# Kernel optimization log

Hardware: AMD Instinct MI355X
Metric: run time of the kernel (lower is better)

Reference implementation:

```python
import jax, jax.numpy as jnp
import numpy as np

EPS = 1e-8  # matches torch F.cosine_similarity eps


def setup_inputs() -> dict:
    key = jax.random.key(0)
    k1, k2, k3 = jax.random.split(key, 3)
    S, B, H = 16, 512, 2048
    OGLogits = jax.random.normal(k1, (B, H), dtype=jnp.float32)
    enhancedSamplesLogits = jax.random.normal(k2, (S, B, H), dtype=jnp.float32)
    W = jax.random.normal(k3, (H, H), dtype=jnp.float32) * (1.0 / np.sqrt(H))
    b = jnp.zeros((H,), dtype=jnp.float32)
    return {"OGLogits": OGLogits, "enhancedSamplesLogits": enhancedSamplesLogits, "W": W, "b": b}


def reference(OGLogits, enhancedSamplesLogits, W, b):
    # Original torch code builds the full (S*B, B) cosine-similarity matrix and
    # keeps only the diagonal via an eye mask; mathematically that equals the
    # per-pair cosine similarity cos(enhanced[s,b], OG[b]), computed directly here.
    e_norm = jnp.linalg.norm(enhancedSamplesLogits, axis=-1)          # (S, B)
    o_norm = jnp.linalg.norm(OGLogits, axis=-1)                       # (B,)
    dots = jnp.einsum('sbh,bh->sb', enhancedSamplesLogits, OGLogits)  # (S, B)
    sims = dots / jnp.maximum(e_norm * o_norm[None, :], EPS)          # (S, B)
    weighted = enhancedSamplesLogits * sims[..., None]                # (S, B, H)
    weightedRep = weighted.mean(axis=0)                               # (B, H)
    return weightedRep @ W.T + b                                      # (B, H)
```

## Files before the change

kernel.cpp:

```cpp
#include <hip/hip_runtime.h>

#define S_DIM 16
#define B_DIM 512
#define H_DIM 2048
#define EPS 1e-8f

typedef short bf16x8 __attribute__((ext_vector_type(8)));
typedef float f32x16 __attribute__((ext_vector_type(16)));

__device__ __forceinline__ unsigned short f2bf(float f) {
    union { float f; unsigned int u; } v; v.f = f;
    unsigned int u = v.u;
    unsigned int r = (u + 0x7fffu + ((u >> 16) & 1u)) >> 16;
    return (unsigned short)r;
}

__device__ __forceinline__ float dot4(const float4& a, const float4& b) {
    return a.x*b.x + a.y*b.y + a.z*b.z + a.w*b.w;
}

__global__ __launch_bounds__(512, 4) void fused_kernel(
    const float* __restrict__ OG, const float* __restrict__ E,
    const float* __restrict__ W, unsigned short* __restrict__ wrep,
    unsigned short* __restrict__ Wb) {
    const int b = blockIdx.x;
    const int t = threadIdx.x;
    const int lane = t & 63;
    const int wave = t >> 6;

    __shared__ float4 buf[8][512];
    __shared__ float4 ogs[512];
    __shared__ float red[8];

    const float4* w4 = (const float4*)W;
    ushort4* wb4 = (ushort4*)Wb;
    const size_t wbase = (size_t)b * 2048 + t;

    float4 wv0 = w4[wbase];
    float4 wv1 = w4[wbase + 512];
    const float4* og4 = (const float4*)(OG + (size_t)b * H_DIM);
    float4 o = og4[t];

    const float4* e4a = (const float4*)(E + ((size_t)wave * B_DIM + b) * H_DIM);
    const float4* e4b = (const float4*)(E + ((size_t)(wave + 8) * B_DIM + b) * H_DIM);
    float4 ea[8], eb[8];
    #pragma unroll
    for (int i = 0; i < 8; ++i) {
        ea[i] = e4a[i * 64 + lane];
        eb[i] = e4b[i * 64 + lane];
    }
    float4 wv2 = w4[wbase + 1024];
    float4 wv3 = w4[wbase + 1536];

    ogs[t] = o;
    float p = dot4(o, o);
    #pragma unroll
    for (int m = 32; m >= 1; m >>= 1) p += __shfl_xor(p, m, 64);
    if (lane == 0) red[wave] = p;

    {
        ushort4 c0, c1;
        c0.x = f2bf(wv0.x); c0.y = f2bf(wv0.y); c0.z = f2bf(wv0.z); c0.w = f2bf(wv0.w);
        c1.x = f2bf(wv1.x); c1.y = f2bf(wv1.y); c1.z = f2bf(wv1.z); c1.w = f2bf(wv1.w);
        wb4[wbase] = c0;
        wb4[wbase + 512] = c1;
    }
    __syncthreads();

    float og2 = 0.f;
    #pragma unroll
    for (int w = 0; w < 8; ++w) og2 += red[w];
    const float onorm = sqrtf(og2);

    float da = 0.f, na = 0.f, db = 0.f, nb = 0.f;
    #pragma unroll
    for (int i = 0; i < 8; ++i) {
        float4 g = ogs[i * 64 + lane];
        da += dot4(ea[i], g); na += dot4(ea[i], ea[i]);
        db += dot4(eb[i], g); nb += dot4(eb[i], eb[i]);
    }
    #pragma unroll
    for (int m = 32; m >= 1; m >>= 1) {
        da += __shfl_xor(da, m, 64);
        na += __shfl_xor(na, m, 64);
        db += __shfl_xor(db, m, 64);
        nb += __shfl_xor(nb, m, 64);
    }
    const float sima = da / fmaxf(sqrtf(na) * onorm, EPS);
    const float simb = db / fmaxf(sqrtf(nb) * onorm, EPS);

    #pragma unroll
    for (int i = 0; i < 8; ++i) {
        float4 v;
        v.x = ea[i].x * sima + eb[i].x * simb;
        v.y = ea[i].y * sima + eb[i].y * simb;
        v.z = ea[i].z * sima + eb[i].z * simb;
        v.w = ea[i].w * sima + eb[i].w * simb;
        buf[wave][i * 64 + lane] = v;
    }
    {
        ushort4 c2, c3;
        c2.x = f2bf(wv2.x); c2.y = f2bf(wv2.y); c2.z = f2bf(wv2.z); c2.w = f2bf(wv2.w);
        c3.x = f2bf(wv3.x); c3.y = f2bf(wv3.y); c3.z = f2bf(wv3.z); c3.w = f2bf(wv3.w);
        wb4[wbase + 1024] = c2;
        wb4[wbase + 1536] = c3;
    }
    __syncthreads();

    float4 s = buf[0][t];
    #pragma unroll
    for (int w = 1; w < 8; ++w) {
        float4 v = buf[w][t];
        s.x += v.x; s.y += v.y; s.z += v.z; s.w += v.w;
    }
    const float sc = 1.f / (float)S_DIM;
    ushort4 ob;
    ob.x = f2bf(s.x * sc); ob.y = f2bf(s.y * sc);
    ob.z = f2bf(s.z * sc); ob.w = f2bf(s.w * sc);
    ((ushort4*)wrep)[(size_t)b * (H_DIM / 4) + t] = ob;
}

__global__ __launch_bounds__(256) void gemm_kernel(
    const unsigned short* __restrict__ A, const unsigned short* __restrict__ Wb,
    const float* __restrict__ bias, float* __restrict__ out) {
    const int bid = blockIdx.x;
    const int m0 = (bid & 7) * 64;
    const int n0 = (bid >> 3) * 64;

    __shared__ unsigned short As[2][64 * 72];
    __shared__ unsigned short Bs[2][64 * 72];

    const int t = threadIdx.x;
    const int lane = t & 63;
    const int wave = t >> 6;
    const int wm = (wave & 1) * 32;
    const int wn = (wave >> 1) * 32;

    const int lr = t >> 2, lq = t & 3;
    const unsigned short* ap = A  + (size_t)(m0 + lr) * H_DIM + lq * 16;
    const unsigned short* bp = Wb + (size_t)(n0 + lr) * H_DIM + lq * 16;

    const int sw = (lr & 7) << 4;
    const int w0 = lr * 72 + (((lq * 32) ^ sw) >> 1);
    const int w1 = lr * 72 + (((lq * 32 + 16) ^ sw) >> 1);

    f32x16 acc0 = {0.f,0.f,0.f,0.f,0.f,0.f,0.f,0.f,
                   0.f,0.f,0.f,0.f,0.f,0.f,0.f,0.f};
    f32x16 acc1 = {0.f,0.f,0.f,0.f,0.f,0.f,0.f,0.f,
                   0.f,0.f,0.f,0.f,0.f,0.f,0.f,0.f};

    const int row = lane & 31;
    const int hi = lane >> 5;
    const int rbase = (wm + row) * 72;
    const int rsw = ((row & 7) << 4);
    int roffA[4], roffB[4];
    #pragma unroll
    for (int ks = 0; ks < 4; ++ks) {
        const int x = (ks * 32 + hi * 16) ^ rsw;
        roffA[ks] = rbase + (x >> 1);
        roffB[ks] = (wn + row) * 72 + (x >> 1);
    }

    uint4 ra0 = *(const uint4*)(ap);
    uint4 ra1 = *(const uint4*)(ap + 8);
    uint4 rb0 = *(const uint4*)(bp);
    uint4 rb1 = *(const uint4*)(bp + 8);
    uint4 sa0 = *(const uint4*)(ap + 64);
    uint4 sa1 = *(const uint4*)(ap + 72);
    uint4 sb0 = *(const uint4*)(bp + 64);
    uint4 sb1 = *(const uint4*)(bp + 72);
    *(uint4*)&As[0][w0] = ra0;
    *(uint4*)&As[0][w1] = ra1;
    *(uint4*)&Bs[0][w0] = rb0;
    *(uint4*)&Bs[0][w1] = rb1;
    __syncthreads();

    #define MFMA_TILE(BUF)                                                        \
    {                                                                             \
        _Pragma("unroll")                                                         \
        for (int ks = 0; ks < 2; ++ks) {                                          \
            bf16x8 afA = *(const bf16x8*)&As[BUF][roffA[ks]];                     \
            bf16x8 bfA = *(const bf16x8*)&Bs[BUF][roffB[ks]];                     \
            acc0 = __builtin_amdgcn_mfma_f32_32x32x16_bf16(afA, bfA, acc0, 0,0,0);\
            bf16x8 afB = *(const bf16x8*)&As[BUF][roffA[ks + 2]];                 \
            bf16x8 bfB = *(const bf16x8*)&Bs[BUF][roffB[ks + 2]];                 \
            acc1 = __builtin_amdgcn_mfma_f32_32x32x16_bf16(afB, bfB, acc1, 0,0,0);\
        }                                                                         \
    }

    for (int ki = 0; ki < 32; ki += 2) {
        if (ki + 2 < 32) {
            ra0 = *(const uint4*)(ap + (ki + 2) * 64);
            ra1 = *(const uint4*)(ap + (ki + 2) * 64 + 8);
            rb0 = *(const uint4*)(bp + (ki + 2) * 64);
            rb1 = *(const uint4*)(bp + (ki + 2) * 64 + 8);
        }
        MFMA_TILE(0);
        *(uint4*)&As[1][w0] = sa0;
        *(uint4*)&As[1][w1] = sa1;
        *(uint4*)&Bs[1][w0] = sb0;
        *(uint4*)&Bs[1][w1] = sb1;
        __syncthreads();
        if (ki + 3 < 32) {
            sa0 = *(const uint4*)(ap + (ki + 3) * 64);
            sa1 = *(const uint4*)(ap + (ki + 3) * 64 + 8);
            sb0 = *(const uint4*)(bp + (ki + 3) * 64);
            sb1 = *(const uint4*)(bp + (ki + 3) * 64 + 8);
        }
        MFMA_TILE(1);
        if (ki + 2 < 32) {
            *(uint4*)&As[0][w0] = ra0;
            *(uint4*)&As[0][w1] = ra1;
            *(uint4*)&Bs[0][w0] = rb0;
            *(uint4*)&Bs[0][w1] = rb1;
            __syncthreads();
        }
    }
    #undef MFMA_TILE

    const int col = lane & 31;
    const float bias0 = bias[n0 + wn + col];
    #pragma unroll
    for (int r = 0; r < 16; ++r) {
        const int mr = (r & 3) + 8 * (r >> 2) + 4 * hi;
        out[(size_t)(m0 + wm + mr) * H_DIM + n0 + wn + col] = acc0[r] + acc1[r] + bias0;
    }
}

extern "C" void kernel_launch(void* const* d_in, const int* in_sizes, int n_in,
                              void* d_out, int out_size, void* d_ws, size_t ws_size,
                              hipStream_t stream) {
    const float* OG   = (const float*)d_in[0];
    const float* E    = (const float*)d_in[1];
    const float* W    = (const float*)d_in[2];
    const float* bias = (const float*)d_in[3];
    float* out = (float*)d_out;

    unsigned short* wrep = (unsigned short*)d_ws;
    unsigned short* Wb   = wrep + (size_t)B_DIM * H_DIM;

    fused_kernel<<<B_DIM, 512, 0, stream>>>(OG, E, W, wrep, Wb);
    gemm_kernel<<<256, 256, 0, stream>>>(wrep, Wb, bias, out);
}
```

Before: 124.8 us.

## Restructure GEMM with direct global-to-LDS loads, split-K waves and XCD-aware tiling

Rewrites the bf16 GEMM so each wave computes the full 64x64 tile over a quarter of each K-slice, which gives four MFMAs per wave per step from two A and two B fragments. Partial sums are then reduced across the four waves through shared memory. Tiles are staged with global_load_lds, skipping the register round trip, and blocks are remapped so each XCD shares N columns of W. The cost is a large LDS reduction buffer (64KB) and a barrier every K step.

```diff
diff --git a/kernel.cpp b/kernel.cpp
--- a/kernel.cpp
+++ b/kernel.cpp
@@ -124,106 +124,98 @@
     const unsigned short* __restrict__ A, const unsigned short* __restrict__ Wb,
     const float* __restrict__ bias, float* __restrict__ out) {
     const int bid = blockIdx.x;
-    const int m0 = (bid & 7) * 64;
-    const int n0 = (bid >> 3) * 64;
-
-    __shared__ unsigned short As[2][64 * 72];
-    __shared__ unsigned short Bs[2][64 * 72];
+    const int xcd = bid & 7, j = bid >> 3;
+    const int n0 = (xcd * 4 + (j & 3)) * 64;
+    const int m0 = (j >> 2) * 64;
+
+    __shared__ unsigned short As[2][64 * 64];
+    __shared__ unsigned short Bs[2][64 * 64];
+    __shared__ float red[4][16][256];
 
     const int t = threadIdx.x;
     const int lane = t & 63;
-    const int wave = t >> 6;
-    const int wm = (wave & 1) * 32;
-    const int wn = (wave >> 1) * 32;
-
-    const int lr = t >> 2, lq = t & 3;
-    const unsigned short* ap = A  + (size_t)(m0 + lr) * H_DIM + lq * 16;
-    const unsigned short* bp = Wb + (size_t)(n0 + lr) * H_DIM + lq * 16;
-
-    const int sw = (lr & 7) << 4;
-    const int w0 = lr * 72 + (((lq * 32) ^ sw) >> 1);
-    const int w1 = lr * 72 + (((lq * 32 + 16) ^ sw) >> 1);
-
-    f32x16 acc0 = {0.f,0.f,0.f,0.f,0.f,0.f,0.f,0.f,
-                   0.f,0.f,0.f,0.f,0.f,0.f,0.f,0.f};
-    f32x16 acc1 = {0.f,0.f,0.f,0.f,0.f,0.f,0.f,0.f,
-                   0.f,0.f,0.f,0.f,0.f,0.f,0.f,0.f};
+    const int kh = t >> 6;
+
+    const int srow0 = t >> 3;
+    const int srow1 = srow0 + 32;
+    const int colb = (t & 7) << 4;
+    const int sc0 = colb ^ ((srow0 & 7) << 4);
+    const int sc1 = colb ^ ((srow1 & 7) << 4);
+    const unsigned short* apg0 = A  + (size_t)(m0 + srow0) * H_DIM + (sc0 >> 1);
+    const unsigned short* apg1 = A  + (size_t)(m0 + srow1) * H_DIM + (sc1 >> 1);
+    const unsigned short* bpg0 = Wb + (size_t)(n0 + srow0) * H_DIM + (sc0 >> 1);
+    const unsigned short* bpg1 = Wb + (size_t)(n0 + srow1) * H_DIM + (sc1 >> 1);
+
+    #define GLL(SRC, DST)                                                   \
+        __builtin_amdgcn_global_load_lds(                                   \
+            (const __attribute__((address_space(1))) unsigned int*)(const void*)(SRC), \
+            (__attribute__((address_space(3))) unsigned int*)(void*)(DST),  \
+            16, 0, 0)
+    #define STAGE(BUF, KI)                                  \
+        do {                                                \
+            GLL(apg0 + (KI) * 64, &As[BUF][t * 8]);         \
+            GLL(apg1 + (KI) * 64, &As[BUF][2048 + t * 8]);  \
+            GLL(bpg0 + (KI) * 64, &Bs[BUF][t * 8]);         \
+            GLL(bpg1 + (KI) * 64, &Bs[BUF][2048 + t * 8]);  \
+        } while (0)
 
     const int row = lane & 31;
     const int hi = lane >> 5;
-    const int rbase = (wm + row) * 72;
-    const int rsw = ((row & 7) << 4);
-    int roffA[4], roffB[4];
-    #pragma unroll
-    for (int ks = 0; ks < 4; ++ks) {
-        const int x = (ks * 32 + hi * 16) ^ rsw;
-        roffA[ks] = rbase + (x >> 1);
-        roffB[ks] = (wn + row) * 72 + (x >> 1);
-    }
-
-    uint4 ra0 = *(const uint4*)(ap);
-    uint4 ra1 = *(const uint4*)(ap + 8);
-    uint4 rb0 = *(const uint4*)(bp);
-    uint4 rb1 = *(const uint4*)(bp + 8);
-    uint4 sa0 = *(const uint4*)(ap + 64);
-    uint4 sa1 = *(const uint4*)(ap + 72);
-    uint4 sb0 = *(const uint4*)(bp + 64);
-    uint4 sb1 = *(const uint4*)(bp + 72);
-    *(uint4*)&As[0][w0] = ra0;
-    *(uint4*)&As[0][w1] = ra1;
-    *(uint4*)&Bs[0][w0] = rb0;
-    *(uint4*)&Bs[0][w1] = rb1;
-    __syncthreads();
-
-    #define MFMA_TILE(BUF)                                                        \
-    {                                                                             \
-        _Pragma("unroll")                                                         \
-        for (int ks = 0; ks < 2; ++ks) {                                          \
-            bf16x8 afA = *(const bf16x8*)&As[BUF][roffA[ks]];                     \
-            bf16x8 bfA = *(const bf16x8*)&Bs[BUF][roffB[ks]];                     \
-            acc0 = __builtin_amdgcn_mfma_f32_32x32x16_bf16(afA, bfA, acc0, 0,0,0);\
-            bf16x8 afB = *(const bf16x8*)&As[BUF][roffA[ks + 2]];                 \
-            bf16x8 bfB = *(const bf16x8*)&Bs[BUF][roffB[ks + 2]];                 \
-            acc1 = __builtin_amdgcn_mfma_f32_32x32x16_bf16(afB, bfB, acc1, 0,0,0);\
-        }                                                                         \
-    }
-
-    for (int ki = 0; ki < 32; ki += 2) {
-        if (ki + 2 < 32) {
-            ra0 = *(const uint4*)(ap + (ki + 2) * 64);
-            ra1 = *(const uint4*)(ap + (ki + 2) * 64 + 8);
-            rb0 = *(const uint4*)(bp + (ki + 2) * 64);
-            rb1 = *(const uint4*)(bp + (ki + 2) * 64 + 8);
+    const int off0 = row * 64 + ((((kh * 32 + hi * 16)) ^ ((row & 7) << 4)) >> 1);
+
+    f32x16 acc0 = {0.f,0.f,0.f,0.f,0.f,0.f,0.f,0.f,0.f,0.f,0.f,0.f,0.f,0.f,0.f,0.f};
+    f32x16 acc1 = acc0, acc2 = acc0, acc3 = acc0;
+
+    STAGE(0, 0);
+    __syncthreads();
+
+    for (int ki = 0; ki < 32; ++ki) {
+        const int cur = ki & 1;
+        if (ki + 1 < 32) STAGE(cur ^ 1, ki + 1);
+        bf16x8 a0 = *(const bf16x8*)&As[cur][off0];
+        bf16x8 a1 = *(const bf16x8*)&As[cur][off0 + 2048];
+        bf16x8 b0 = *(const bf16x8*)&Bs[cur][off0];
+        bf16x8 b1 = *(const bf16x8*)&Bs[cur][off0 + 2048];
+        acc0 = __builtin_amdgcn_mfma_f32_32x32x16_bf16(a0, b0, acc0, 0, 0, 0);
+        acc1 = __builtin_amdgcn_mfma_f32_32x32x16_bf16(a0, b1, acc1, 0, 0, 0);
+        acc2 = __builtin_amdgcn_mfma_f32_32x32x16_bf16(a1, b0, acc2, 0, 0, 0);
+        acc3 = __builtin_amdgcn_mfma_f32_32x32x16_bf16(a1, b1, acc3, 0, 0, 0);
+        __syncthreads();
+    }
+    #undef STAGE
+    #undef GLL
+
+    #define DUMP(C, ACC)                                                     \
+        { _Pragma("unroll")                                                  \
+          for (int r4 = 0; r4 < 4; ++r4) {                                   \
+              float4 v = {(ACC)[r4*4], (ACC)[r4*4+1], (ACC)[r4*4+2], (ACC)[r4*4+3]}; \
+              *(float4*)&red[kh][(C)*4 + r4][lane << 2] = v;                 \
+          } }
+    DUMP(0, acc0); DUMP(1, acc1); DUMP(2, acc2); DUMP(3, acc3);
+    #undef DUMP
+    __syncthreads();
+
+    const int qm = kh >> 1, qn = kh & 1;
+    const int col = n0 + qn * 32 + row;
+    const float bias0 = bias[col];
+    #pragma unroll
+    for (int i = 0; i < 4; ++i) {
+        const int s = kh * 4 + i;
+        float4 v0 = *(float4*)&red[0][s][lane << 2];
+        float4 v1 = *(float4*)&red[1][s][lane << 2];
+        float4 v2 = *(float4*)&red[2][s][lane << 2];
+        float4 v3 = *(float4*)&red[3][s][lane << 2];
+        float4 v;
+        v.x = v0.x + v1.x + v2.x + v3.x;
+        v.y = v0.y + v1.y + v2.y + v3.y;
+        v.z = v0.z + v1.z + v2.z + v3.z;
+        v.w = v0.w + v1.w + v2.w + v3.w;
+        const float vv[4] = {v.x, v.y, v.z, v.w};
+        #pragma unroll
+        for (int rr = 0; rr < 4; ++rr) {
+            const int mr = rr + 8 * i + 4 * hi;
+            out[(size_t)(m0 + qm * 32 + mr) * H_DIM + col] = vv[rr] + bias0;
         }
-        MFMA_TILE(0);
-        *(uint4*)&As[1][w0] = sa0;
-        *(uint4*)&As[1][w1] = sa1;
-        *(uint4*)&Bs[1][w0] = sb0;
-        *(uint4*)&Bs[1][w1] = sb1;
-        __syncthreads();
-        if (ki + 3 < 32) {
-            sa0 = *(const uint4*)(ap + (ki + 3) * 64);
-            sa1 = *(const uint4*)(ap + (ki + 3) * 64 + 8);
-            sb0 = *(const uint4*)(bp + (ki + 3) * 64);
-            sb1 = *(const uint4*)(bp + (ki + 3) * 64 + 8);
-        }
-        MFMA_TILE(1);
-        if (ki + 2 < 32) {
-            *(uint4*)&As[0][w0] = ra0;
-            *(uint4*)&As[0][w1] = ra1;
-            *(uint4*)&Bs[0][w0] = rb0;
-            *(uint4*)&Bs[0][w1] = rb1;
-            __syncthreads();
-        }
-    }
-    #undef MFMA_TILE
-
-    const int col = lane & 31;
-    const float bias0 = bias[n0 + wn + col];
-    #pragma unroll
-    for (int r = 0; r < 16; ++r) {
-        const int mr = (r & 3) + 8 * (r >> 2) + 4 * hi;
-        out[(size_t)(m0 + wm + mr) * H_DIM + n0 + wn + col] = acc0[r] + acc1[r] + bias0;
     }
 }
 
```

New measurement: 139.2 us. 11.5% more time.

## Convert W to bf16 inside GEMM tile loads instead of separate pre-pass

Applied to the files above, without the earlier changes.

Removes the fp32-to-bf16 conversion of W from the first kernel, so the GEMM now reads W as fp32 and packs it to bf16 when staging tiles into shared memory. This avoids writing and re-reading a bf16 copy of W through global memory, but the GEMM fetches twice as many bytes for W and redoes the conversion in every block that shares an N tile. It also drops the LDS row padding in favour of the XOR swizzle alone, and remaps block indices so the blocks sharing an N tile of W land on the same XCD, improving L2 reuse of W.

```diff
diff --git a/kernel.cpp b/kernel.cpp
--- a/kernel.cpp
+++ b/kernel.cpp
@@ -15,14 +15,20 @@
     return (unsigned short)r;
 }
 
+__device__ __forceinline__ uint4 pack8(const float4 a, const float4 b) {
+    union { unsigned short u[8]; uint4 v; } r;
+    r.u[0] = f2bf(a.x); r.u[1] = f2bf(a.y); r.u[2] = f2bf(a.z); r.u[3] = f2bf(a.w);
+    r.u[4] = f2bf(b.x); r.u[5] = f2bf(b.y); r.u[6] = f2bf(b.z); r.u[7] = f2bf(b.w);
+    return r.v;
+}
+
 __device__ __forceinline__ float dot4(const float4& a, const float4& b) {
     return a.x*b.x + a.y*b.y + a.z*b.z + a.w*b.w;
 }
 
 __global__ __launch_bounds__(512, 4) void fused_kernel(
     const float* __restrict__ OG, const float* __restrict__ E,
-    const float* __restrict__ W, unsigned short* __restrict__ wrep,
-    unsigned short* __restrict__ Wb) {
+    unsigned short* __restrict__ wrep) {
     const int b = blockIdx.x;
     const int t = threadIdx.x;
     const int lane = t & 63;
@@ -32,12 +38,6 @@
     __shared__ float4 ogs[512];
     __shared__ float red[8];
 
-    const float4* w4 = (const float4*)W;
-    ushort4* wb4 = (ushort4*)Wb;
-    const size_t wbase = (size_t)b * 2048 + t;
-
-    float4 wv0 = w4[wbase];
-    float4 wv1 = w4[wbase + 512];
     const float4* og4 = (const float4*)(OG + (size_t)b * H_DIM);
     float4 o = og4[t];
 
@@ -49,22 +49,12 @@
         ea[i] = e4a[i * 64 + lane];
         eb[i] = e4b[i * 64 + lane];
     }
-    float4 wv2 = w4[wbase + 1024];
-    float4 wv3 = w4[wbase + 1536];
 
     ogs[t] = o;
     float p = dot4(o, o);
     #pragma unroll
     for (int m = 32; m >= 1; m >>= 1) p += __shfl_xor(p, m, 64);
     if (lane == 0) red[wave] = p;
-
-    {
-        ushort4 c0, c1;
-        c0.x = f2bf(wv0.x); c0.y = f2bf(wv0.y); c0.z = f2bf(wv0.z); c0.w = f2bf(wv0.w);
-        c1.x = f2bf(wv1.x); c1.y = f2bf(wv1.y); c1.z = f2bf(wv1.z); c1.w = f2bf(wv1.w);
-        wb4[wbase] = c0;
-        wb4[wbase + 512] = c1;
-    }
     __syncthreads();
 
     float og2 = 0.f;
@@ -98,13 +88,6 @@
         v.w = ea[i].w * sima + eb[i].w * simb;
         buf[wave][i * 64 + lane] = v;
     }
-    {
-        ushort4 c2, c3;
-        c2.x = f2bf(wv2.x); c2.y = f2bf(wv2.y); c2.z = f2bf(wv2.z); c2.w = f2bf(wv2.w);
-        c3.x = f2bf(wv3.x); c3.y = f2bf(wv3.y); c3.z = f2bf(wv3.z); c3.w = f2bf(wv3.w);
-        wb4[wbase + 1024] = c2;
-        wb4[wbase + 1536] = c3;
-    }
     __syncthreads();
 
     float4 s = buf[0][t];
@@ -121,14 +104,15 @@
 }
 
 __global__ __launch_bounds__(256) void gemm_kernel(
-    const unsigned short* __restrict__ A, const unsigned short* __restrict__ Wb,
+    const unsigned short* __restrict__ A, const float* __restrict__ W,
     const float* __restrict__ bias, float* __restrict__ out) {
     const int bid = blockIdx.x;
-    const int m0 = (bid & 7) * 64;
-    const int n0 = (bid >> 3) * 64;
-
-    __shared__ unsigned short As[2][64 * 72];
-    __shared__ unsigned short Bs[2][64 * 72];
+    const int xcd = bid & 7, j = bid >> 3;
+    const int n0 = (xcd * 4 + (j & 3)) * 64;
+    const int m0 = (j >> 2) * 64;
+
+    __shared__ unsigned short As[2][64 * 64];
+    __shared__ unsigned short Bs[2][64 * 64];
 
     const int t = threadIdx.x;
     const int lane = t & 63;
@@ -137,42 +121,44 @@
     const int wn = (wave >> 1) * 32;
 
     const int lr = t >> 2, lq = t & 3;
-    const unsigned short* ap = A  + (size_t)(m0 + lr) * H_DIM + lq * 16;
-    const unsigned short* bp = Wb + (size_t)(n0 + lr) * H_DIM + lq * 16;
-
-    const int sw = (lr & 7) << 4;
-    const int w0 = lr * 72 + (((lq * 32) ^ sw) >> 1);
-    const int w1 = lr * 72 + (((lq * 32 + 16) ^ sw) >> 1);
+    const unsigned short* ap = A + (size_t)(m0 + lr) * H_DIM + lq * 16;
+    const float*          wp = W + (size_t)(n0 + lr) * H_DIM + lq * 16;
+
+    const int swz = (lr & 7) << 4;
+    const int w0 = lr * 64 + (((lq * 32) ^ swz) >> 1);
+    const int w1 = lr * 64 + (((lq * 32 + 16) ^ swz) >> 1);
 
     f32x16 acc0 = {0.f,0.f,0.f,0.f,0.f,0.f,0.f,0.f,
                    0.f,0.f,0.f,0.f,0.f,0.f,0.f,0.f};
-    f32x16 acc1 = {0.f,0.f,0.f,0.f,0.f,0.f,0.f,0.f,
-                   0.f,0.f,0.f,0.f,0.f,0.f,0.f,0.f};
+    f32x16 acc1 = acc0;
 
     const int row = lane & 31;
     const int hi = lane >> 5;
-    const int rbase = (wm + row) * 72;
-    const int rsw = ((row & 7) << 4);
+    const int rswz = (row & 7) << 4;
     int roffA[4], roffB[4];
     #pragma unroll
     for (int ks = 0; ks < 4; ++ks) {
-        const int x = (ks * 32 + hi * 16) ^ rsw;
-        roffA[ks] = rbase + (x >> 1);
-        roffB[ks] = (wn + row) * 72 + (x >> 1);
-    }
-
-    uint4 ra0 = *(const uint4*)(ap);
-    uint4 ra1 = *(const uint4*)(ap + 8);
-    uint4 rb0 = *(const uint4*)(bp);
-    uint4 rb1 = *(const uint4*)(bp + 8);
-    uint4 sa0 = *(const uint4*)(ap + 64);
-    uint4 sa1 = *(const uint4*)(ap + 72);
-    uint4 sb0 = *(const uint4*)(bp + 64);
-    uint4 sb1 = *(const uint4*)(bp + 72);
+        const int x = ((ks * 32 + hi * 16) ^ rswz) >> 1;
+        roffA[ks] = (wm + row) * 64 + x;
+        roffB[ks] = (wn + row) * 64 + x;
+    }
+
+    uint4  ra0 = *(const uint4*)(ap);
+    uint4  ra1 = *(const uint4*)(ap + 8);
+    float4 rf0 = *(const float4*)(wp);
+    float4 rf1 = *(const float4*)(wp + 4);
+    float4 rf2 = *(const float4*)(wp + 8);
+    float4 rf3 = *(const float4*)(wp + 12);
+    uint4  sa0 = *(const uint4*)(ap + 64);
+    uint4  sa1 = *(const uint4*)(ap + 72);
+    float4 sf0 = *(const float4*)(wp + 64);
+    float4 sf1 = *(const float4*)(wp + 68);
+    float4 sf2 = *(const float4*)(wp + 72);
+    float4 sf3 = *(const float4*)(wp + 76);
     *(uint4*)&As[0][w0] = ra0;
     *(uint4*)&As[0][w1] = ra1;
-    *(uint4*)&Bs[0][w0] = rb0;
-    *(uint4*)&Bs[0][w1] = rb1;
+    *(uint4*)&Bs[0][w0] = pack8(rf0, rf1);
+    *(uint4*)&Bs[0][w1] = pack8(rf2, rf3);
     __syncthreads();
 
     #define MFMA_TILE(BUF)                                                        \
@@ -192,27 +178,31 @@
         if (ki + 2 < 32) {
             ra0 = *(const uint4*)(ap + (ki + 2) * 64);
             ra1 = *(const uint4*)(ap + (ki + 2) * 64 + 8);
-            rb0 = *(const uint4*)(bp + (ki + 2) * 64);
-            rb1 = *(const uint4*)(bp + (ki + 2) * 64 + 8);
+            rf0 = *(const float4*)(wp + (ki + 2) * 64);
+            rf1 = *(const float4*)(wp + (ki + 2) * 64 + 4);
+            rf2 = *(const float4*)(wp + (ki + 2) * 64 + 8);
+            rf3 = *(const float4*)(wp + (ki + 2) * 64 + 12);
         }
         MFMA_TILE(0);
         *(uint4*)&As[1][w0] = sa0;
         *(uint4*)&As[1][w1] = sa1;
-        *(uint4*)&Bs[1][w0] = sb0;
-        *(uint4*)&Bs[1][w1] = sb1;
+        *(uint4*)&Bs[1][w0] = pack8(sf0, sf1);
+        *(uint4*)&Bs[1][w1] = pack8(sf2, sf3);
         __syncthreads();
         if (ki + 3 < 32) {
             sa0 = *(const uint4*)(ap + (ki + 3) * 64);
             sa1 = *(const uint4*)(ap + (ki + 3) * 64 + 8);
-            sb0 = *(const uint4*)(bp + (ki + 3) * 64);
-            sb1 = *(const uint4*)(bp + (ki + 3) * 64 + 8);
+            sf0 = *(const float4*)(wp + (ki + 3) * 64);
+            sf1 = *(const float4*)(wp + (ki + 3) * 64 + 4);
+            sf2 = *(const float4*)(wp + (ki + 3) * 64 + 8);
+            sf3 = *(const float4*)(wp + (ki + 3) * 64 + 12);
         }
         MFMA_TILE(1);
         if (ki + 2 < 32) {
             *(uint4*)&As[0][w0] = ra0;
             *(uint4*)&As[0][w1] = ra1;
-            *(uint4*)&Bs[0][w0] = rb0;
-            *(uint4*)&Bs[0][w1] = rb1;
+            *(uint4*)&Bs[0][w0] = pack8(rf0, rf1);
+            *(uint4*)&Bs[0][w1] = pack8(rf2, rf3);
             __syncthreads();
         }
     }
@@ -237,8 +227,7 @@
     float* out = (float*)d_out;
 
     unsigned short* wrep = (unsigned short*)d_ws;
-    unsigned short* Wb   = wrep + (size_t)B_DIM * H_DIM;
-
-    fused_kernel<<<B_DIM, 512, 0, stream>>>(OG, E, W, wrep, Wb);
-    gemm_kernel<<<256, 256, 0, stream>>>(wrep, Wb, bias, out);
-}
+
+    fused_kernel<<<B_DIM, 512, 0, stream>>>(OG, E, wrep);
+    gemm_kernel<<<256, 256, 0, stream>>>(wrep, W, bias, out);
+}
```

Result: slower. 137.2 us (+10.0%).
